# Kernel tuning notes

Measured on AMD Instinct MI355X. Metric: run time of the kernel, lower is better.

## Reference

```python
import jax, jax.numpy as jnp
import numpy as np

B = 4096
OBS, ACT, RDIM = 128, 32, 4
HID = 1024                      # embedding output / head hidden dim
DIMS = [OBS + ACT + RDIM, 128, 128, RDIM]   # target net: 164 -> 128 -> 128 -> 4
N_LAYERS = len(DIMS) - 1


def setup_inputs() -> dict:
    key = jax.random.key(0)
    ks = iter(jax.random.split(key, 64))

    def p(shape, scale=0.02):
        return jax.random.normal(next(ks), shape, jnp.float32) * scale

    inp = {
        "obs": jax.random.normal(next(ks), (B, OBS), jnp.float32),
        "action": jax.random.normal(next(ks), (B, ACT), jnp.float32),
        "prefs": jax.random.uniform(next(ks), (B, RDIM), jnp.float32),
        # embedding MLP (hypernet): (obs, prefs) -> z
        "We1": p((OBS + RDIM, HID)), "be1": jnp.zeros((HID,), jnp.float32),
        "We2": p((HID, HID)), "be2": jnp.zeros((HID,), jnp.float32),
    }
    # head nets: per target layer, linear heads emitting weight / bias / scale
    for i in range(N_LAYERS):
        din, dout = DIMS[i], DIMS[i + 1]
        inp[f"Ww{i}"] = p((HID, dout * din))
        inp[f"bw{i}"] = jnp.zeros((dout * din,), jnp.float32)
        inp[f"Wb{i}"] = p((HID, dout))
        inp[f"bb{i}"] = jnp.zeros((dout,), jnp.float32)
        inp[f"Ws{i}"] = p((HID, dout))
        inp[f"bs{i}"] = jnp.ones((dout,), jnp.float32)  # scale ~ 1 at init
    return inp


def reference(obs, action, prefs, We1, be1, We2, be2,
              Ww0, bw0, Wb0, bb0, Ws0, bs0,
              Ww1, bw1, Wb1, bb1, Ws1, bs1,
              Ww2, bw2, Wb2, bb2, Ws2, bs2):
    # hypernet embedding z  (hypernet_inputs = [obs, prefs])
    hin = jnp.concatenate([obs, prefs], axis=-1)          # [B, 132]
    z = jax.nn.relu(hin @ We1 + be1)
    z = jax.nn.relu(z @ We2 + be2)                        # [B, HID]

    heads = [(Ww0, bw0, Wb0, bb0, Ws0, bs0),
             (Ww1, bw1, Wb1, bb1, Ws1, bs1),
             (Ww2, bw2, Wb2, bb2, Ws2, bs2)]

    # target network input (target_net_inputs = [obs, action, prefs])
    x = jnp.concatenate([obs, action, prefs], axis=-1)    # [B, 164]

    for i, (Ww, bw, Wb, bb, Ws, bs) in enumerate(heads):
        din, dout = DIMS[i], DIMS[i + 1]
        w = (z @ Ww + bw).reshape(-1, dout, din)          # per-sample [B, dout, din]
        b = z @ Wb + bb                                   # [B, dout]
        s = z @ Ws + bs                                   # [B, dout]
        x = (jnp.einsum('bi,boi->bo', x, w) + b) * s      # batched matmul+bias+scale
        if i < N_LAYERS - 1:                              # activation_mask: all but last
            x = jax.nn.relu(x)
    return x                                              # [B, reward_dim]
```

## Files before the change

### kernel.cpp

```cpp
#include <hip/hip_runtime.h>
#include <hip/hip_bf16.h>
#include <stdint.h>

#define B4 4096
#define KZ 1056
#define KH 160

typedef short bf16x8 __attribute__((ext_vector_type(8)));
typedef float f32x4 __attribute__((ext_vector_type(4)));

__device__ __forceinline__ float b2f(uint16_t u){
  union {float f; uint32_t i;} v; v.i = ((uint32_t)u)<<16; return v.f;
}
__device__ __forceinline__ uint16_t f2b(float f){
  union {float fv; uint32_t i;} v; v.fv = f;
  uint32_t r = v.i + 0x7FFFu + ((v.i>>16)&1u);
  return (uint16_t)(r>>16);
}
__device__ __forceinline__ void gload16(const void* g, void* l){
  __builtin_amdgcn_global_load_lds(
      (__attribute__((address_space(1))) void*)(g),
      (__attribute__((address_space(3))) void*)(l), 16, 0, 0);
}

__device__ __forceinline__ void tp_tile(
    float (*tile)[33],
    const float* __restrict__ src, const float* __restrict__ bias,
    uint16_t* __restrict__ dst,
    int Ncols, int Kdst, int Ksrc, int src_ld, int din_dst, int din_src,
    int ct, int kt)
{
  int tid = threadIdx.x;
  int cl = tid & 31, kg = tid >> 5;
  #pragma unroll
  for (int r = 0; r < 4; ++r){
    int kl = kg*4 + r;
    int k  = kt*32 + kl;
    int c  = ct*32 + cl;
    float v = 0.f;
    if (c < Ncols){
      int o = c / din_dst, i = c - o*din_dst;
      if (i < din_src){
        int sc = o*din_src + i;
        if (k < Ksrc)       v = src[(size_t)k*src_ld + sc];
        else if (k == Ksrc) v = bias[sc];
      }
    }
    tile[kl][cl] = v;
  }
  __syncthreads();
  int c_loc = tid >> 3, kq = tid & 7;
  int c = ct*32 + c_loc;
  if (c < Ncols){
    ushort4 st;
    uint16_t* sp = (uint16_t*)&st;
    #pragma unroll
    for (int r = 0; r < 4; ++r) sp[r] = f2b(tile[kq*4 + r][c_loc]);
    *(ushort4*)&dst[(size_t)c*Kdst + kt*32 + kq*4] = st;
  }
}

__global__ __launch_bounds__(256) void mega_prep(
    const float* __restrict__ Ww0, const float* __restrict__ bw0,
    const float* __restrict__ Ww1, const float* __restrict__ bw1,
    const float* __restrict__ Ww2, const float* __restrict__ bw2,
    const float* __restrict__ We1, const float* __restrict__ be1,
    const float* __restrict__ We2, const float* __restrict__ be2,
    const float* __restrict__ Wb0, const float* __restrict__ bb0,
    const float* __restrict__ Ws0, const float* __restrict__ bs0,
    const float* __restrict__ Wb1, const float* __restrict__ bb1,
    const float* __restrict__ Ws1, const float* __restrict__ bs1,
    const float* __restrict__ Wb2, const float* __restrict__ bb2,
    const float* __restrict__ Ws2, const float* __restrict__ bs2,
    const float* __restrict__ obs, const float* __restrict__ act,
    const float* __restrict__ prefs,
    uint16_t* __restrict__ WpT0, uint16_t* __restrict__ WpT1,
    uint16_t* __restrict__ WpT2, uint16_t* __restrict__ We1T,
    uint16_t* __restrict__ We2T, uint16_t* __restrict__ WbsT,
    uint16_t* __restrict__ Wbs2T,
    uint16_t* __restrict__ hinp, uint16_t* __restrict__ x0T,
    uint16_t* __restrict__ z1p, uint16_t* __restrict__ zp)
{
  __shared__ float tile[32][33];
  int bid = blockIdx.x;
  int tid = threadIdx.x;

  if (bid < 25344){
    tp_tile(tile, Ww0, bw0, WpT0, 24576, KZ, 1024, 20992, 192, 164,
            bid % 768, bid / 768);
  } else if (bid < 42240){
    int b = bid - 25344;
    tp_tile(tile, Ww1, bw1, WpT1, 16384, KZ, 1024, 16384, 128, 128,
            b % 512, b / 512);
  } else if (bid < 42768){
    int b = bid - 42240;
    tp_tile(tile, Ww2, bw2, WpT2, 512, KZ, 1024, 512, 128, 128,
            b % 16, b / 16);
  } else if (bid < 42928){
    int b = bid - 42768;
    tp_tile(tile, We1, be1, We1T, 1024, KH, 132, 1024, 1024, 1024,
            b % 32, b / 32);
  } else if (bid < 43984){
    int b = bid - 42928;
    tp_tile(tile, We2, be2, We2T, 1024, KZ, 1024, 1024, 1024, 1024,
            b % 32, b / 32);
  } else if (bid < 44545){
    int b = bid - 43984;
    int ct = b % 17, kt = b / 17;
    int cl = tid & 31, kg = tid >> 5;
    #pragma unroll
    for (int r = 0; r < 4; ++r){
      int kl = kg*4 + r;
      int k  = kt*32 + kl;
      int c  = ct*32 + cl;
      float v = 0.f;
      if (c < 512){
        int sel = c >> 7, sc = c & 127;
        const float* S  = (sel==0) ? Wb0 : (sel==1) ? Ws0 : (sel==2) ? Wb1 : Ws1;
        const float* Bs = (sel==0) ? bb0 : (sel==1) ? bs0 : (sel==2) ? bb1 : bs1;
        if (k < 1024)       v = S[(size_t)k*128 + sc];
        else if (k == 1024) v = Bs[sc];
      } else if (c < 520){
        int cc = c - 512;
        int sel = cc >> 2, sc = cc & 3;
        const float* S  = sel ? Ws2 : Wb2;
        const float* Bs = sel ? bs2 : bb2;
        if (k < 1024)       v = S[(size_t)k*4 + sc];
        else if (k == 1024) v = Bs[sc];
      }
      tile[kl][cl] = v;
    }
    __syncthreads();
    int c_loc = tid >> 3, kq = tid & 7;
    int c = ct*32 + c_loc;
    if (c < 520){
      ushort4 st;
      uint16_t* sp = (uint16_t*)&st;
      #pragma unroll
      for (int r = 0; r < 4; ++r) sp[r] = f2b(tile[kq*4 + r][c_loc]);
      uint16_t* dst = (c < 512) ? &WbsT[(size_t)c*KZ] : &Wbs2T[(size_t)(c-512)*KZ];
      *(ushort4*)&dst[kt*32 + kq*4] = st;
    }
  } else {
    int b = bid - 44545;
    if (b < 2560){
      int idx = b*256 + tid;
      int bb = idx / KH, k = idx - bb*KH;
      float v;
      if (k < 128)      v = obs[bb*128 + k];
      else if (k < 132) v = prefs[bb*4 + (k-128)];
      else              v = (k == 132) ? 1.f : 0.f;
      hinp[idx] = f2b(v);
    } else if (b < 5632){
      int idx = (b-2560)*256 + tid;
      int c = idx >> 12;
      int bb = idx & (B4-1);
      float v = 0.f;
      if (c < 128)      v = obs[bb*128 + c];
      else if (c < 160) v = act[bb*32 + (c-128)];
      else if (c < 164) v = prefs[bb*4 + (c-160)];
      x0T[idx] = f2b(v);
    } else {
      int idx = (b-5632)*256 + tid;
      int t = idx & 63;
      int row = idx >> 6;
      uint16_t* p = (t < 32) ? z1p : zp;
      int col = 1024 + (t & 31);
      p[(size_t)row*KZ + col] = ((t & 31) == 0) ? (uint16_t)0x3F80 : (uint16_t)0;
    }
  }
}

template<int RELU, int OUTBF, int TRANS>
__global__ __launch_bounds__(256) void gemm128(
    const uint16_t* __restrict__ A, int lda,
    const uint16_t* __restrict__ BT, int ldb,
    void* __restrict__ Cv, int ldc, int K)
{
  __shared__ char smA[128*64];
  __shared__ char smB[128*64];
  int tid = threadIdx.x, w = tid >> 6, lane = tid & 63;
  int m0 = blockIdx.x*128, n0 = blockIdx.y*128;
  const uint16_t* Ab = A  + (size_t)m0*lda;
  const uint16_t* Bb = BT + (size_t)n0*ldb;
  f32x4 acc[2][8];
  #pragma unroll
  for (int mf = 0; mf < 2; ++mf)
    #pragma unroll
    for (int nf = 0; nf < 8; ++nf) acc[mf][nf] = (f32x4){0.f,0.f,0.f,0.f};
  int colg = lane & 15, hi = lane >> 4;

  for (int k0 = 0; k0 < K; k0 += 32){
    #pragma unroll
    for (int p = 0; p < 2; ++p){
      int rb = p*4 + w;
      int row = rb*16 + (lane >> 2);
      int chunk = (lane & 3) ^ ((row >> 1) & 3);
      gload16(Ab + (size_t)row*lda + k0 + chunk*8, &smA[rb*1024]);
      gload16(Bb + (size_t)row*ldb + k0 + chunk*8, &smB[rb*1024]);
    }
    __syncthreads();
    bf16x8 af[2];
    #pragma unroll
    for (int mf = 0; mf < 2; ++mf){
      int row = w*32 + mf*16 + colg;
      af[mf] = *(const bf16x8*)&smA[row*64 + ((hi ^ ((row>>1)&3)) << 4)];
    }
    #pragma unroll
    for (int nf = 0; nf < 8; ++nf){
      int row = nf*16 + colg;
      bf16x8 bfr = *(const bf16x8*)&smB[row*64 + ((hi ^ ((row>>1)&3)) << 4)];
      acc[0][nf] = __builtin_amdgcn_mfma_f32_16x16x32_bf16(af[0], bfr, acc[0][nf], 0,0,0);
      acc[1][nf] = __builtin_amdgcn_mfma_f32_16x16x32_bf16(af[1], bfr, acc[1][nf], 0,0,0);
    }
    __syncthreads();
  }
  #pragma unroll
  for (int mf = 0; mf < 2; ++mf){
    #pragma unroll
    for (int nf = 0; nf < 8; ++nf){
      int col = n0 + nf*16 + colg;
      #pragma unroll
      for (int r = 0; r < 4; ++r){
        int row = m0 + w*32 + mf*16 + hi*4 + r;
        float v = acc[mf][nf][r];
        if (RELU) v = v > 0.f ? v : 0.f;
        if (TRANS)      ((float*)Cv)[(size_t)col*ldc + row] = v;
        else if (OUTBF) ((uint16_t*)Cv)[(size_t)row*ldc + col] = f2b(v);
        else            ((float*)Cv)[(size_t)row*ldc + col] = v;
      }
    }
  }
}

__global__ __launch_bounds__(256) void gemm_heads(
    const uint16_t* __restrict__ zp, const uint16_t* __restrict__ Wbs0T,
    const uint16_t* __restrict__ Wbs2T, const uint16_t* __restrict__ WpT2,
    float* __restrict__ bsb0, float* __restrict__ bsb2, float* __restrict__ w2)
{
  __shared__ char smA[128*64];
  __shared__ char smB[128*64];
  int y = blockIdx.y;
  const uint16_t* BT; float* Cv; int ldc, n0, trans;
  if (y < 4)      { BT = Wbs0T; Cv = bsb0; ldc = B4;  n0 = y*128;     trans = 1; }
  else if (y == 4){ BT = Wbs2T; Cv = bsb2; ldc = 128; n0 = 0;         trans = 0; }
  else            { BT = WpT2;  Cv = w2;   ldc = 512; n0 = (y-5)*128; trans = 0; }

  int tid = threadIdx.x, w = tid >> 6, lane = tid & 63;
  int m0 = blockIdx.x*128;
  const uint16_t* Ab = zp + (size_t)m0*KZ;
  const uint16_t* Bb = BT + (size_t)n0*KZ;
  f32x4 acc[2][8];
  #pragma unroll
  for (int mf = 0; mf < 2; ++mf)
    #pragma unroll
    for (int nf = 0; nf < 8; ++nf) acc[mf][nf] = (f32x4){0.f,0.f,0.f,0.f};
  int colg = lane & 15, hi = lane >> 4;

  for (int k0 = 0; k0 < KZ; k0 += 32){
    #pragma unroll
    for (int p = 0; p < 2; ++p){
      int rb = p*4 + w;
      int row = rb*16 + (lane >> 2);
      int chunk = (lane & 3) ^ ((row >> 1) & 3);
      gload16(Ab + (size_t)row*KZ + k0 + chunk*8, &smA[rb*1024]);
      gload16(Bb + (size_t)row*KZ + k0 + chunk*8, &smB[rb*1024]);
    }
    __syncthreads();
    bf16x8 af[2];
    #pragma unroll
    for (int mf = 0; mf < 2; ++mf){
      int row = w*32 + mf*16 + colg;
      af[mf] = *(const bf16x8*)&smA[row*64 + ((hi ^ ((row>>1)&3)) << 4)];
    }
    #pragma unroll
    for (int nf = 0; nf < 8; ++nf){
      int row = nf*16 + colg;
      bf16x8 bfr = *(const bf16x8*)&smB[row*64 + ((hi ^ ((row>>1)&3)) << 4)];
      acc[0][nf] = __builtin_amdgcn_mfma_f32_16x16x32_bf16(af[0], bfr, acc[0][nf], 0,0,0);
      acc[1][nf] = __builtin_amdgcn_mfma_f32_16x16x32_bf16(af[1], bfr, acc[1][nf], 0,0,0);
    }
    __syncthreads();
  }
  #pragma unroll
  for (int mf = 0; mf < 2; ++mf){
    #pragma unroll
    for (int nf = 0; nf < 8; ++nf){
      int col = n0 + nf*16 + colg;
      #pragma unroll
      for (int r = 0; r < 4; ++r){
        int row = m0 + w*32 + mf*16 + hi*4 + r;
        float v = acc[mf][nf][r];
        if (trans) Cv[(size_t)col*ldc + row] = v;
        else       Cv[(size_t)row*ldc + col] = v;
      }
    }
  }
}

template<int DINP>
__global__ __launch_bounds__(512, 2) void hyper2n(
    const uint16_t* __restrict__ zp,
    const uint16_t* __restrict__ WpT,
    const uint16_t* __restrict__ xT,
    const float*  __restrict__ bsbT,
    uint16_t* __restrict__ outT,
    int relu)
{
  constexpr int NF     = DINP/32;
  constexpr int BCALLS = DINP/64;
  constexpr int WAITN  = 2 + BCALLS;
  constexpr int HBUF   = 16384 + 2*DINP*64;
  constexpr int NH     = KZ/32;
  __shared__ char sm[3*HBUF];

  int tid = threadIdx.x, w = tid >> 6, lane = tid & 63;
  int wm = w >> 2, wn = w & 3;
  int f = blockIdx.x;
  int xcd = f & 7;
  int j = f >> 3;
  int pair = j >> 1;
  int mt = xcd*2 + (j & 1);
  int m0 = mt*256;
  const uint16_t* Ag = zp  + (size_t)m0*KZ;
  const uint16_t* Bg = WpT + (size_t)pair*(2*DINP)*KZ;
  int colg = lane & 15, hi = lane >> 4;

  f32x4 acc[8][NF];
  #pragma unroll
  for (int mf = 0; mf < 8; ++mf)
    #pragma unroll
    for (int nf = 0; nf < NF; ++nf) acc[mf][nf] = (f32x4){0.f,0.f,0.f,0.f};

  auto SA = [&](int h, int a){
    int row = a*128 + (tid >> 2);
    int ch  = (tid & 3) ^ ((row >> 1) & 3);
    gload16(Ag + (size_t)row*KZ + h*32 + ch*8,
            sm + (h%3)*HBUF + a*8192 + w*1024);
  };
  auto SB = [&](int h, int b){
    int row = b*128 + (tid >> 2);
    int ch  = (tid & 3) ^ ((row >> 1) & 3);
    gload16(Bg + (size_t)row*KZ + h*32 + ch*8,
            sm + (h%3)*HBUF + 16384 + b*8192 + w*1024);
  };

  SA(0,0); SA(0,1);
  #pragma unroll
  for (int b = 0; b < BCALLS; ++b) SB(0,b);
  SA(1,0); SA(1,1);
  #pragma unroll
  for (int b = 0; b < BCALLS; ++b) SB(1,b);

  for (int h = 0; h < NH; ++h){
    const char* base = sm + (h%3)*HBUF;
    if (h == NH-1) asm volatile("s_waitcnt vmcnt(0)" ::: "memory");
    else           asm volatile("s_waitcnt vmcnt(%0)" :: "i"(WAITN) : "memory");
    __builtin_amdgcn_s_barrier();
    if (h + 2 < NH){
      SA(h+2,0); SA(h+2,1);
      #pragma unroll
      for (int b = 0; b < BCALLS; ++b) SB(h+2,b);
    }
    bf16x8 Bf[NF];
    #pragma unroll
    for (int nf = 0; nf < NF; ++nf){
      int rc = wn*(DINP/2) + nf*16 + colg;
      Bf[nf] = *(const bf16x8*)(base + 16384 + rc*64 + ((hi ^ ((rc>>1)&3)) << 4));
    }
    #pragma unroll
    for (int m = 0; m < 8; ++m){
      int row = wm*128 + m*16 + colg;
      bf16x8 a = *(const bf16x8*)(base + row*64 + ((hi ^ ((row>>1)&3)) << 4));
      #pragma unroll
      for (int nf = 0; nf < NF; ++nf)
        acc[m][nf] = __builtin_amdgcn_mfma_f32_16x16x32_bf16(a, Bf[nf], acc[m][nf], 0,0,0);
    }
  }

  __syncthreads();
  float* red = (float*)sm;
  int parity = wn & 1, o_loc = wn >> 1;
  #pragma unroll
  for (int mf = 0; mf < 8; ++mf){
    float p0=0.f, p1=0.f, p2=0.f, p3=0.f;
    int b0 = m0 + wm*128 + mf*16 + hi*4;
    #pragma unroll
    for (int nf = 0; nf < NF; ++nf){
      int il = parity*(DINP/2) + nf*16 + colg;
      ushort4 xv = *(const ushort4*)(xT + (size_t)il*B4 + b0);
      f32x4 a = acc[mf][nf];
      p0 += a[0]*b2f(xv.x); p1 += a[1]*b2f(xv.y);
      p2 += a[2]*b2f(xv.z); p3 += a[3]*b2f(xv.w);
    }
    #pragma unroll
    for (int off = 1; off < 16; off <<= 1){
      p0 += __shfl_xor(p0, off); p1 += __shfl_xor(p1, off);
      p2 += __shfl_xor(p2, off); p3 += __shfl_xor(p3, off);
    }
    if (colg == 0){
      int rloc = wm*128 + mf*16 + hi*4;
      float* rp = red + parity*512 + o_loc*256 + rloc;
      rp[0] = p0; rp[1] = p1; rp[2] = p2; rp[3] = p3;
    }
  }
  __syncthreads();
  {
    int o_l = tid >> 8, row = tid & 255;
    int o = pair*2 + o_l;
    float v = red[o_l*256 + row] + red[512 + o_l*256 + row];
    float bv = bsbT[(size_t)o*B4 + m0 + row];
    float sv = bsbT[(size_t)(128+o)*B4 + m0 + row];
    float val = (v + bv) * sv;
    if (relu) val = val > 0.f ? val : 0.f;
    outT[(size_t)o*B4 + m0 + row] = f2b(val);
  }
}

__global__ __launch_bounds__(256) void finalize_k(
    const float* __restrict__ w2, const uint16_t* __restrict__ x2T,
    const float* __restrict__ bs2, float* __restrict__ out)
{
  int tid = threadIdx.x;
  int o = tid & 3;
  int b = blockIdx.x*64 + (tid >> 2);
  const float* wr = w2 + (size_t)b*512 + o*128;
  float dot = 0.f;
  #pragma unroll
  for (int i = 0; i < 128; i += 4){
    float4 wv = *(const float4*)(wr + i);
    dot += wv.x * b2f(x2T[(size_t)(i+0)*B4 + b]);
    dot += wv.y * b2f(x2T[(size_t)(i+1)*B4 + b]);
    dot += wv.z * b2f(x2T[(size_t)(i+2)*B4 + b]);
    dot += wv.w * b2f(x2T[(size_t)(i+3)*B4 + b]);
  }
  float bv = bs2[(size_t)b*128 + o];
  float sv = bs2[(size_t)b*128 + 4 + o];
  out[b*4 + o] = (dot + bv) * sv;
}

extern "C" void kernel_launch(void* const* d_in, const int* in_sizes, int n_in,
                              void* d_out, int out_size, void* d_ws, size_t ws_size,
                              hipStream_t stream)
{
  const float* obs   = (const float*)d_in[0];
  const float* act   = (const float*)d_in[1];
  const float* prefs = (const float*)d_in[2];
  const float* We1 = (const float*)d_in[3];
  const float* be1 = (const float*)d_in[4];
  const float* We2 = (const float*)d_in[5];
  const float* be2 = (const float*)d_in[6];
  const float* Ww0 = (const float*)d_in[7],  *bw0 = (const float*)d_in[8];
  const float* Wb0 = (const float*)d_in[9],  *bb0 = (const float*)d_in[10];
  const float* Ws0 = (const float*)d_in[11], *bs0i = (const float*)d_in[12];
  const float* Ww1 = (const float*)d_in[13], *bw1 = (const float*)d_in[14];
  const float* Wb1 = (const float*)d_in[15], *bb1 = (const float*)d_in[16];
  const float* Ws1 = (const float*)d_in[17], *bs1i = (const float*)d_in[18];
  const float* Ww2 = (const float*)d_in[19], *bw2 = (const float*)d_in[20];
  const float* Wb2 = (const float*)d_in[21], *bb2 = (const float*)d_in[22];
  const float* Ws2 = (const float*)d_in[23], *bs2i = (const float*)d_in[24];

  char* ws = (char*)d_ws;
  size_t off = 0;
  auto alloc = [&](size_t bytes)->char*{
    char* p = ws + off; off += (bytes + 255) & ~(size_t)255; return p;
  };
  uint16_t* WpT0  = (uint16_t*)alloc((size_t)24576*KZ*2);
  uint16_t* WpT1  = (uint16_t*)alloc((size_t)16384*KZ*2);
  uint16_t* WpT2  = (uint16_t*)alloc((size_t)512*KZ*2);
  uint16_t* We1T  = (uint16_t*)alloc((size_t)1024*KH*2);
  uint16_t* We2T  = (uint16_t*)alloc((size_t)1024*KZ*2);
  uint16_t* Wbs0T = (uint16_t*)alloc((size_t)256*KZ*2);
  uint16_t* Wbs1T = (uint16_t*)alloc((size_t)256*KZ*2);
  uint16_t* Wbs2T = (uint16_t*)alloc((size_t)128*KZ*2);
  uint16_t* hinp  = (uint16_t*)alloc((size_t)B4*KH*2);
  uint16_t* z1p   = (uint16_t*)alloc((size_t)B4*KZ*2);
  uint16_t* zp    = (uint16_t*)alloc((size_t)B4*KZ*2);
  float*    bsb0  = (float*)alloc((size_t)256*B4*4);
  float*    bsb1  = (float*)alloc((size_t)256*B4*4);
  float*    bsb2  = (float*)alloc((size_t)B4*128*4);
  uint16_t* x0T   = (uint16_t*)alloc((size_t)192*B4*2);
  uint16_t* x1T   = (uint16_t*)alloc((size_t)128*B4*2);
  uint16_t* x2T   = (uint16_t*)alloc((size_t)128*B4*2);
  float*    w2    = (float*)alloc((size_t)B4*512*4);
  (void)ws_size; (void)in_sizes; (void)n_in; (void)out_size;
  (void)Wbs1T;

  hipMemsetAsync(Wbs2T, 0, (size_t)128*KZ*2, stream);

  dim3 blk(256);
  mega_prep<<<dim3(51201),blk,0,stream>>>(
      Ww0, bw0, Ww1, bw1, Ww2, bw2, We1, be1, We2, be2,
      Wb0, bb0, Ws0, bs0i, Wb1, bb1, Ws1, bs1i, Wb2, bb2, Ws2, bs2i,
      obs, act, prefs,
      WpT0, WpT1, WpT2, We1T, We2T, Wbs0T, Wbs2T,
      hinp, x0T, z1p, zp);

  gemm128<1,1,0><<<dim3(32,8),blk,0,stream>>>(hinp, KH, We1T, KH, z1p, KZ, KH);
  gemm128<1,1,0><<<dim3(32,8),blk,0,stream>>>(z1p, KZ, We2T, KZ, zp, KZ, KZ);
  gemm_heads<<<dim3(32,9),blk,0,stream>>>(zp, Wbs0T, Wbs2T, WpT2, bsb0, bsb2, w2);

  hyper2n<192><<<dim3(1024),dim3(512),0,stream>>>(zp, WpT0, x0T, bsb0, x1T, 1);
  hyper2n<128><<<dim3(1024),dim3(512),0,stream>>>(zp, WpT1, x1T, bsb1, x2T, 1);

  finalize_k<<<dim3(B4/64),blk,0,stream>>>(w2, x2T, bsb2, (float*)d_out);
}
```

Measured before the change: 506.6 us.

## Overlap big head-weight transposes with second embedding GEMM in one launch

Moves the large Ww0/Ww1 fp32-to-bf16 transpose tiles out of the first prep kernel into a new kernel that also runs the z1@We2 GEMM. The GEMM blocks are the first 256 block indices, so they get scheduled early, and the memory-bound transpose tiles fill the remaining CUs. This aims to hide the small GEMM's underutilisation behind bandwidth-heavy conversion work and to shrink the prep kernel so the first GEMM can start sooner. The shared-memory buffer is reused across the two roles, and correctness relies on the WpT0/WpT1 consumers running later in the stream.

```diff
diff --git a/kernel.cpp b/kernel.cpp
--- a/kernel.cpp
+++ b/kernel.cpp
@@ -60,12 +60,10 @@
   }
 }
 
-__global__ __launch_bounds__(256) void mega_prep(
-    const float* __restrict__ Ww0, const float* __restrict__ bw0,
-    const float* __restrict__ Ww1, const float* __restrict__ bw1,
-    const float* __restrict__ Ww2, const float* __restrict__ bw2,
+__global__ __launch_bounds__(256) void prep_small(
     const float* __restrict__ We1, const float* __restrict__ be1,
     const float* __restrict__ We2, const float* __restrict__ be2,
+    const float* __restrict__ Ww2, const float* __restrict__ bw2,
     const float* __restrict__ Wb0, const float* __restrict__ bb0,
     const float* __restrict__ Ws0, const float* __restrict__ bs0,
     const float* __restrict__ Wb1, const float* __restrict__ bb1,
@@ -74,9 +72,8 @@
     const float* __restrict__ Ws2, const float* __restrict__ bs2,
     const float* __restrict__ obs, const float* __restrict__ act,
     const float* __restrict__ prefs,
-    uint16_t* __restrict__ WpT0, uint16_t* __restrict__ WpT1,
-    uint16_t* __restrict__ WpT2, uint16_t* __restrict__ We1T,
-    uint16_t* __restrict__ We2T, uint16_t* __restrict__ WbsT,
+    uint16_t* __restrict__ We1T, uint16_t* __restrict__ We2T,
+    uint16_t* __restrict__ WpT2, uint16_t* __restrict__ WbsT,
     uint16_t* __restrict__ Wbs2T,
     uint16_t* __restrict__ hinp, uint16_t* __restrict__ x0T,
     uint16_t* __restrict__ z1p, uint16_t* __restrict__ zp)
@@ -85,27 +82,19 @@
   int bid = blockIdx.x;
   int tid = threadIdx.x;
 
-  if (bid < 25344){
-    tp_tile(tile, Ww0, bw0, WpT0, 24576, KZ, 1024, 20992, 192, 164,
-            bid % 768, bid / 768);
-  } else if (bid < 42240){
-    int b = bid - 25344;
-    tp_tile(tile, Ww1, bw1, WpT1, 16384, KZ, 1024, 16384, 128, 128,
-            b % 512, b / 512);
-  } else if (bid < 42768){
-    int b = bid - 42240;
+  if (bid < 160){
+    tp_tile(tile, We1, be1, We1T, 1024, KH, 132, 1024, 1024, 1024,
+            bid % 32, bid / 32);
+  } else if (bid < 1216){
+    int b = bid - 160;
+    tp_tile(tile, We2, be2, We2T, 1024, KZ, 1024, 1024, 1024, 1024,
+            b % 32, b / 32);
+  } else if (bid < 1744){
+    int b = bid - 1216;
     tp_tile(tile, Ww2, bw2, WpT2, 512, KZ, 1024, 512, 128, 128,
             b % 16, b / 16);
-  } else if (bid < 42928){
-    int b = bid - 42768;
-    tp_tile(tile, We1, be1, We1T, 1024, KH, 132, 1024, 1024, 1024,
-            b % 32, b / 32);
-  } else if (bid < 43984){
-    int b = bid - 42928;
-    tp_tile(tile, We2, be2, We2T, 1024, KZ, 1024, 1024, 1024, 1024,
-            b % 32, b / 32);
-  } else if (bid < 44545){
-    int b = bid - 43984;
+  } else if (bid < 2305){
+    int b = bid - 1744;
     int ct = b % 17, kt = b / 17;
     int cl = tid & 31, kg = tid >> 5;
     #pragma unroll
@@ -142,7 +131,7 @@
       *(ushort4*)&dst[kt*32 + kq*4] = st;
     }
   } else {
-    int b = bid - 44545;
+    int b = bid - 2305;
     if (b < 2560){
       int idx = b*256 + tid;
       int bb = idx / KH, k = idx - bb*KH;
@@ -230,6 +219,81 @@
         else            ((float*)Cv)[(size_t)row*ldc + col] = v;
       }
     }
+  }
+}
+
+__global__ __launch_bounds__(256) void fused_zw(
+    const uint16_t* __restrict__ z1p, const uint16_t* __restrict__ We2T,
+    uint16_t* __restrict__ zp,
+    const float* __restrict__ Ww0, const float* __restrict__ bw0,
+    uint16_t* __restrict__ WpT0,
+    const float* __restrict__ Ww1, const float* __restrict__ bw1,
+    uint16_t* __restrict__ WpT1)
+{
+  __shared__ char sm[16384];
+  int bid = blockIdx.x;
+  int tid = threadIdx.x;
+
+  if (bid < 256){
+    char* smA = sm; char* smB = sm + 8192;
+    int w = tid >> 6, lane = tid & 63;
+    int m0 = (bid >> 3)*128, n0 = (bid & 7)*128;
+    const uint16_t* Ab = z1p  + (size_t)m0*KZ;
+    const uint16_t* Bb = We2T + (size_t)n0*KZ;
+    f32x4 acc[2][8];
+    #pragma unroll
+    for (int mf = 0; mf < 2; ++mf)
+      #pragma unroll
+      for (int nf = 0; nf < 8; ++nf) acc[mf][nf] = (f32x4){0.f,0.f,0.f,0.f};
+    int colg = lane & 15, hi = lane >> 4;
+
+    for (int k0 = 0; k0 < KZ; k0 += 32){
+      #pragma unroll
+      for (int p = 0; p < 2; ++p){
+        int rb = p*4 + w;
+        int row = rb*16 + (lane >> 2);
+        int chunk = (lane & 3) ^ ((row >> 1) & 3);
+        gload16(Ab + (size_t)row*KZ + k0 + chunk*8, &smA[rb*1024]);
+        gload16(Bb + (size_t)row*KZ + k0 + chunk*8, &smB[rb*1024]);
+      }
+      __syncthreads();
+      bf16x8 af[2];
+      #pragma unroll
+      for (int mf = 0; mf < 2; ++mf){
+        int row = w*32 + mf*16 + colg;
+        af[mf] = *(const bf16x8*)&smA[row*64 + ((hi ^ ((row>>1)&3)) << 4)];
+      }
+      #pragma unroll
+      for (int nf = 0; nf < 8; ++nf){
+        int row = nf*16 + colg;
+        bf16x8 bfr = *(const bf16x8*)&smB[row*64 + ((hi ^ ((row>>1)&3)) << 4)];
+        acc[0][nf] = __builtin_amdgcn_mfma_f32_16x16x32_bf16(af[0], bfr, acc[0][nf], 0,0,0);
+        acc[1][nf] = __builtin_amdgcn_mfma_f32_16x16x32_bf16(af[1], bfr, acc[1][nf], 0,0,0);
+      }
+      __syncthreads();
+    }
+    #pragma unroll
+    for (int mf = 0; mf < 2; ++mf){
+      #pragma unroll
+      for (int nf = 0; nf < 8; ++nf){
+        int col = n0 + nf*16 + colg;
+        #pragma unroll
+        for (int r = 0; r < 4; ++r){
+          int row = m0 + w*32 + mf*16 + hi*4 + r;
+          float v = acc[mf][nf][r];
+          v = v > 0.f ? v : 0.f;
+          zp[(size_t)row*KZ + col] = f2b(v);
+        }
+      }
+    }
+  } else if (bid < 25600){
+    int b = bid - 256;
+    tp_tile((float(*)[33])sm, Ww0, bw0, WpT0, 24576, KZ, 1024, 20992, 192, 164,
+            b % 768, b / 768);
+  } else {
+    int b = bid - 25600;
+    tp_tile((float(*)[33])sm, Ww1, bw1, WpT1, 16384, KZ, 1024, 16384, 128, 128,
+            b % 512, b / 512);
   }
 }
 
@@ -489,15 +553,18 @@
   hipMemsetAsync(Wbs2T, 0, (size_t)128*KZ*2, stream);
 
   dim3 blk(256);
-  mega_prep<<<dim3(51201),blk,0,stream>>>(
-      Ww0, bw0, Ww1, bw1, Ww2, bw2, We1, be1, We2, be2,
+  prep_small<<<dim3(8961),blk,0,stream>>>(
+      We1, be1, We2, be2, Ww2, bw2,
       Wb0, bb0, Ws0, bs0i, Wb1, bb1, Ws1, bs1i, Wb2, bb2, Ws2, bs2i,
       obs, act, prefs,
-      WpT0, WpT1, WpT2, We1T, We2T, Wbs0T, Wbs2T,
+      We1T, We2T, WpT2, Wbs0T, Wbs2T,
       hinp, x0T, z1p, zp);
 
   gemm128<1,1,0><<<dim3(32,8),blk,0,stream>>>(hinp, KH, We1T, KH, z1p, KZ, KH);
-  gemm128<1,1,0><<<dim3(32,8),blk,0,stream>>>(z1p, KZ, We2T, KZ, zp, KZ, KZ);
+
+  fused_zw<<<dim3(42496),blk,0,stream>>>(z1p, We2T, zp,
+                                         Ww0, bw0, WpT0, Ww1, bw1, WpT1);
+
   gemm_heads<<<dim3(32,9),blk,0,stream>>>(zp, Wbs0T, Wbs2T, WpT2, bsb0, bsb2, w2);
 
   hyper2n<192><<<dim3(1024),dim3(512),0,stream>>>(zp, WpT0, x0T, bsb0, x1T, 1);
```

Measured after the change: 558.9 us. 1.1x slower.
